# Performance work log

Hardware: AMD Instinct MI355X
Metric: run time of the kernel (lower is better)

The kernel has to match this reference:

```python
import jax, jax.numpy as jnp
import numpy as np
from jax import lax

B, C, T = 16, 1, 2097152
DS = 16  # downsample_factor


def setup_inputs() -> dict:
    key = jax.random.key(0)
    audio = jax.random.normal(key, (B, C, T), dtype=jnp.float32) * 0.5
    sr, attack_ms, release_ms = 44100.0, 10.0, 100.0
    tc = float(np.exp(-np.log10(9.0)))  # exp(-log10(9)) time-constant numerator
    return {
        'audio': audio,
        'threshold': jnp.array([-20.0], jnp.float32),
        'ratio': jnp.array([4.0], jnp.float32),
        'makeup': jnp.array([3.0], jnp.float32),
        'attack_time': jnp.array([tc / (sr * attack_ms * 0.001 * DS)], jnp.float32),
        'release_time': jnp.array([tc / (sr * release_ms * 0.001 * DS)], jnp.float32),
    }


def _linear_downsample(x, factor):
    # F.interpolate(mode='linear', align_corners=False, scale_factor=1/factor)
    Tin = x.shape[-1]
    Tout = Tin // factor
    scale = Tin / Tout
    src = (jnp.arange(Tout, dtype=jnp.float32) + 0.5) * scale - 0.5
    src = jnp.clip(src, 0.0, Tin - 1)
    x0 = jnp.floor(src).astype(jnp.int32)
    x1 = jnp.minimum(x0 + 1, Tin - 1)
    w = src - x0.astype(jnp.float32)
    return x[..., x0] * (1.0 - w) + x[..., x1] * w


def _upsample_with_windows(x, up):
    # x: [B, C, F] framewise envelope; overlap-add with periodic Hann, hop=up
    xb = jnp.concatenate([x, x[..., -1:]], axis=-1)  # add endpoint
    n = jnp.arange(2 * up, dtype=jnp.float32)
    win = 0.5 * (1.0 - jnp.cos(2.0 * jnp.pi * n / (2 * up)))  # torch.hann_window (periodic)
    frames = xb[..., None] * win  # [B, C, F+1, 2*up]
    bsz, ch, nf, fl = frames.shape
    L = (nf - 1) * up + fl
    idx = (jnp.arange(nf)[:, None] * up + jnp.arange(fl)[None, :]).reshape(-1)
    out = jnp.zeros((bsz, ch, L), frames.dtype).at[:, :, idx].add(frames.reshape(bsz, ch, -1))
    return out[:, :, up:-up]


def reference(audio, threshold, ratio, makeup, attack_time, release_time):
    audio_db = 20.0 * jnp.log10(jnp.abs(audio) + 1e-8)
    comp_db = jnp.where(audio_db > threshold,
                        threshold + (audio_db - threshold) / ratio,
                        audio_db)
    gain = comp_db - audio_db  # [B, C, T], static gain reduction in dB (<= 0)
    gd = _linear_downsample(gain, DS)  # [B, C, T//DS]
    # sequential attack/release gain smoothing (one-pole recurrence) over frames
    gd_t = jnp.moveaxis(gd, -1, 0)  # [T//DS, B, C]
    def step(prev, tgt):
        new = jnp.where(tgt >= prev,
                        attack_time * prev + (1.0 - attack_time) * tgt,
                        release_time * prev + (1.0 - release_time) * tgt)
        return new, new
    _, ys = lax.scan(step, gd_t[0], gd_t)
    gs = jnp.moveaxis(ys, 0, -1)  # smoothed gain, [B, C, T//DS]
    gup = _upsample_with_windows(gs, DS)[..., :gain.shape[-1]]
    out_db = audio_db + gup + makeup
    out = 10.0 ** (out_db / 20.0)
    return jnp.where(audio < 0, -out, out)
```

## Files before the change

kernel.cpp:

```cpp
#include <hip/hip_runtime.h>
#include <math.h>

#define B_SZ 16
#define T_LEN 2097152
#define F_LEN (T_LEN / 16)
#define CHUNK 16
#define CPB (F_LEN / CHUNK)
#define NCHUNKS (B_SZ * CPB)
#define NV4 (B_SZ * T_LEN / 4)
#define PRE 16

__device__ __forceinline__ float gain_db(float s, float thr, float slope) {
    float db = 6.0205999132796239f * __log2f(fabsf(s) + 1e-8f);
    float ov = db - thr;
    return ov > 0.0f ? ov * slope : 0.0f;
}

__global__ __launch_bounds__(256) void k_scan(const float* __restrict__ audio,
                                              const float* __restrict__ thr_p,
                                              const float* __restrict__ ratio_p,
                                              const float* __restrict__ at_p,
                                              const float* __restrict__ rt_p,
                                              float2* __restrict__ gsp) {
    int idx = blockIdx.x * 256 + threadIdx.x;
    int b = idx >> 13;
    int c = idx & (CPB - 1);
    int c0 = c << 4;
    const float* Af = audio + (size_t)b * T_LEN;
    const float thr   = thr_p[0];
    const float slope = 1.0f / ratio_p[0] - 1.0f;

    float g[PRE + CHUNK + 1];
#pragma unroll
    for (int i = 0; i < PRE + CHUNK + 1; ++i) {
        int f = c0 - PRE + i;
        f = f < 0 ? 0 : (f > F_LEN - 1 ? F_LEN - 1 : f);
        float t7 = Af[(size_t)f * 16 + 7];
        float t8 = Af[(size_t)f * 16 + 8];
        g[i] = 0.5f * (gain_db(t7, thr, slope) + gain_db(t8, thr, slope));
    }

    const float at = at_p[0], rt = rt_p[0];
    float o[CHUNK + 1];
    float y;
    if (c == 0) {
        y = g[PRE];
        o[0] = y;
#pragma unroll
        for (int i = 1; i < CHUNK + 1; ++i) {
            float t = g[PRE + i];
            y = fmaf((t >= y) ? at : rt, y - t, t);
            o[i] = y;
        }
    } else {
        y = g[0];
#pragma unroll
        for (int i = 1; i < PRE; ++i) {
            float t = g[i];
            y = fmaf((t >= y) ? at : rt, y - t, t);
        }
#pragma unroll
        for (int i = 0; i < CHUNK + 1; ++i) {
            float t = g[PRE + i];
            y = fmaf((t >= y) ? at : rt, y - t, t);
            o[i] = y;
        }
    }
    if (c == CPB - 1) o[CHUNK] = o[CHUNK - 1];

    float2 pr[CHUNK];
#pragma unroll
    for (int i = 0; i < CHUNK; ++i)
        pr[i] = make_float2(o[i], o[i + 1]);
    float4* q4 = reinterpret_cast<float4*>(gsp + (size_t)b * F_LEN + c0);
#pragma unroll
    for (int i = 0; i < CHUNK / 2; ++i)
        q4[i] = reinterpret_cast<float4*>(pr)[i];
}

__global__ __launch_bounds__(256) void k_out(const float4* __restrict__ audio4,
                                             const float2* __restrict__ gsp,
                                             const float* __restrict__ mk_p,
                                             float4* __restrict__ out4) {
    int i = blockIdx.x * 256 + threadIdx.x;
    int t0 = i << 2;
    int b = t0 >> 21;
    int t = t0 & (T_LEN - 1);
    int q = t >> 4;
    int r0 = t & 15;
    float2 gp = gsp[(size_t)b * F_LEN + q];
    float gq = gp.x;
    float d  = gp.y - gp.x;
    const float K   = 0.16609640474436813f;
    const float mkK = mk_p[0] * K;
    float4 x = audio4[i];
    float xs[4] = {x.x, x.y, x.z, x.w};
    float os[4];
#pragma unroll
    for (int j = 0; j < 4; ++j) {
        float cs  = __cosf((float)(r0 + j) * 0.19634954084936207f);
        float wl  = 0.5f - 0.5f * cs;
        float gup = fmaf(d, wl, gq);
        float m   = fabsf(xs[j]) + 1e-8f;
        float v   = m * __builtin_amdgcn_exp2f(fmaf(gup, K, mkK));
        os[j] = (xs[j] < 0.0f) ? -v : v;
    }
    out4[i] = make_float4(os[0], os[1], os[2], os[3]);
}

extern "C" void kernel_launch(void* const* d_in, const int* in_sizes, int n_in,
                              void* d_out, int out_size, void* d_ws, size_t ws_size,
                              hipStream_t stream) {
    const float* audio  = (const float*)d_in[0];
    const float* thr    = (const float*)d_in[1];
    const float* ratio  = (const float*)d_in[2];
    const float* makeup = (const float*)d_in[3];
    const float* at     = (const float*)d_in[4];
    const float* rt     = (const float*)d_in[5];
    float* out = (float*)d_out;

    float2* gsp = (float2*)d_ws;

    k_scan<<<NCHUNKS / 256, 256, 0, stream>>>(audio, thr, ratio, at, rt, gsp);
    k_out<<<NV4 / 256, 256, 0, stream>>>((const float4*)audio, gsp, makeup,
                                         (float4*)out);
}
```

Baseline: 274.9 us.

## Fuse gain scan and output into one kernel with wave-local LDS exchange

Merges the scan and output kernels into one. Each wave loads its 1024 audio samples once, computes frame gains from the held samples using lane shuffles, and runs the chunked recurrence in four lanes with a warm-up prefix through LDS. The output is then applied directly, which removes the global float2 intermediate, a second pass over the audio and one launch. It also replaces the per-sample cosine with precomputed Hann weights. The risks are serialized scan lanes stalling the wave and reliance on wave-level LDS fences instead of __syncthreads.

```diff
diff --git a/kernel.cpp b/kernel.cpp
--- a/kernel.cpp
+++ b/kernel.cpp
@@ -4,108 +4,130 @@
 #define B_SZ 16
 #define T_LEN 2097152
 #define F_LEN (T_LEN / 16)
-#define CHUNK 16
-#define CPB (F_LEN / CHUNK)
-#define NCHUNKS (B_SZ * CPB)
-#define NV4 (B_SZ * T_LEN / 4)
-#define PRE 16
+#define NBLOCKS 8192
+#define K_LOG 0.16609640474436813f
+
+typedef float f32x4 __attribute__((ext_vector_type(4)));
+
+#define KEEP4(v) asm volatile("" :: "v"(v.x), "v"(v.y), "v"(v.z), "v"(v.w))
+#define LGKM_FENCE() asm volatile("s_waitcnt lgkmcnt(0)" ::: "memory")
 
 __device__ __forceinline__ float gain_db(float s, float thr, float slope) {
     float db = 6.0205999132796239f * __log2f(fabsf(s) + 1e-8f);
     float ov = db - thr;
     return ov > 0.0f ? ov * slope : 0.0f;
 }
+__device__ __forceinline__ float step1(float y, float t, float at, float rt) {
+    return fmaf((t >= y) ? at : rt, y - t, t);
+}
+__device__ __forceinline__ float win_sel(int p, float a, float b, float c, float d) {
+    float lo = (p & 1) ? b : a;
+    float hi = (p & 1) ? d : c;
+    return (p & 2) ? hi : lo;
+}
 
-__global__ __launch_bounds__(256) void k_scan(const float* __restrict__ audio,
-                                              const float* __restrict__ thr_p,
-                                              const float* __restrict__ ratio_p,
-                                              const float* __restrict__ at_p,
-                                              const float* __restrict__ rt_p,
-                                              float2* __restrict__ gsp) {
-    int idx = blockIdx.x * 256 + threadIdx.x;
-    int b = idx >> 13;
-    int c = idx & (CPB - 1);
-    int c0 = c << 4;
-    const float* Af = audio + (size_t)b * T_LEN;
+__global__ __launch_bounds__(256) void k_fused(const float4* __restrict__ audio4,
+                                               const float* __restrict__ thr_p,
+                                               const float* __restrict__ ratio_p,
+                                               const float* __restrict__ mk_p,
+                                               const float* __restrict__ at_p,
+                                               const float* __restrict__ rt_p,
+                                               float4* __restrict__ out4) {
+    __shared__ float  gd_s[4][84];
+    __shared__ float2 yp_s[4][64];
+
+    const int tid  = threadIdx.x;
+    const int lane = tid & 63;
+    const int wv   = tid >> 6;
+    const int b    = blockIdx.x >> 9;
+    const int bib  = blockIdx.x & 511;
+    const int W0   = (bib << 8) + (wv << 6);
+
+    const float*  Af = (const float*)audio4 + (size_t)b * T_LEN;
+    const float4* A4 = audio4 + (size_t)b * (T_LEN / 4) + (size_t)W0 * 4;
+    float4*       O4 = out4  + (size_t)b * (T_LEN / 4) + (size_t)W0 * 4;
+
+    float4 xs0 = A4[lane];
+    float4 xs1 = A4[lane + 64];
+    float4 xs2 = A4[lane + 128];
+    float4 xs3 = A4[lane + 192];
+    KEEP4(xs0); KEEP4(xs1); KEEP4(xs2); KEEP4(xs3);
+
+    float t7 = 0.0f, t8 = 0.0f;
+    if (lane < 17) {
+        int fr = (lane < 16) ? (W0 - 16 + lane) : (W0 + 64);
+        fr = fr < 0 ? 0 : (fr > F_LEN - 1 ? F_LEN - 1 : fr);
+        t7 = Af[(size_t)fr * 16 + 7];
+        t8 = Af[(size_t)fr * 16 + 8];
+    }
+
     const float thr   = thr_p[0];
     const float slope = 1.0f / ratio_p[0] - 1.0f;
+    const float at = at_p[0], rt = rt_p[0];
+    const int   p  = lane & 3;
 
-    float g[PRE + CHUNK + 1];
-#pragma unroll
-    for (int i = 0; i < PRE + CHUNK + 1; ++i) {
-        int f = c0 - PRE + i;
-        f = f < 0 ? 0 : (f > F_LEN - 1 ? F_LEN - 1 : f);
-        float t7 = Af[(size_t)f * 16 + 7];
-        float t8 = Af[(size_t)f * 16 + 8];
-        g[i] = 0.5f * (gain_db(t7, thr, slope) + gain_db(t8, thr, slope));
+#define GDJ(J, XV) {                                                   \
+        float v  = (p == 1) ? XV.w : XV.x;                             \
+        float g  = gain_db(v, thr, slope);                             \
+        float gp = __shfl_xor(g, 3);                                   \
+        if (p == 1) gd_s[wv][16 + 16 * J + (lane >> 2)] = 0.5f * (g + gp); }
+    GDJ(0, xs0) GDJ(1, xs1) GDJ(2, xs2) GDJ(3, xs3)
+#undef GDJ
+    if (lane < 17) {
+        float gw = 0.5f * (gain_db(t7, thr, slope) + gain_db(t8, thr, slope));
+        gd_s[wv][(lane < 16) ? lane : 80] = gw;
     }
+    LGKM_FENCE();
 
-    const float at = at_p[0], rt = rt_p[0];
-    float o[CHUNK + 1];
-    float y;
-    if (c == 0) {
-        y = g[PRE];
-        o[0] = y;
-#pragma unroll
-        for (int i = 1; i < CHUNK + 1; ++i) {
-            float t = g[PRE + i];
-            y = fmaf((t >= y) ? at : rt, y - t, t);
-            o[i] = y;
+    if (lane < 4) {
+        const float4* gp4 = reinterpret_cast<const float4*>(&gd_s[wv][16 * lane]);
+        float4 r0 = gp4[0], r1 = gp4[1], r2 = gp4[2], r3 = gp4[3];
+        float4 r4 = gp4[4], r5 = gp4[5], r6 = gp4[6], r7 = gp4[7];
+        float  rE = gd_s[wv][16 * lane + 32];
+        __builtin_amdgcn_sched_barrier(0);
+        bool exact = (bib == 0) && (wv == 0) && (lane == 0);
+        float y;
+        if (exact) {
+            y = r4.x;
+        } else {
+            y = r0.x;
+            y = step1(y, r0.y, at, rt); y = step1(y, r0.z, at, rt); y = step1(y, r0.w, at, rt);
+            y = step1(y, r1.x, at, rt); y = step1(y, r1.y, at, rt); y = step1(y, r1.z, at, rt); y = step1(y, r1.w, at, rt);
+            y = step1(y, r2.x, at, rt); y = step1(y, r2.y, at, rt); y = step1(y, r2.z, at, rt); y = step1(y, r2.w, at, rt);
+            y = step1(y, r3.x, at, rt); y = step1(y, r3.y, at, rt); y = step1(y, r3.z, at, rt); y = step1(y, r3.w, at, rt);
+            y = step1(y, r4.x, at, rt);
         }
-    } else {
-        y = g[0];
-#pragma unroll
-        for (int i = 1; i < PRE; ++i) {
-            float t = g[i];
-            y = fmaf((t >= y) ? at : rt, y - t, t);
-        }
-#pragma unroll
-        for (int i = 0; i < CHUNK + 1; ++i) {
-            float t = g[PRE + i];
-            y = fmaf((t >= y) ? at : rt, y - t, t);
-            o[i] = y;
-        }
+        float2* ypb = &yp_s[wv][16 * lane];
+        float yn;
+#define PAIRSTEP(T, IDX) yn = step1(y, T, at, rt); ypb[IDX] = make_float2(y, yn); y = yn;
+        PAIRSTEP(r4.y, 0)  PAIRSTEP(r4.z, 1)  PAIRSTEP(r4.w, 2)
+        PAIRSTEP(r5.x, 3)  PAIRSTEP(r5.y, 4)  PAIRSTEP(r5.z, 5)  PAIRSTEP(r5.w, 6)
+        PAIRSTEP(r6.x, 7)  PAIRSTEP(r6.y, 8)  PAIRSTEP(r6.z, 9)  PAIRSTEP(r6.w, 10)
+        PAIRSTEP(r7.x, 11) PAIRSTEP(r7.y, 12) PAIRSTEP(r7.z, 13) PAIRSTEP(r7.w, 14)
+        PAIRSTEP(rE, 15)
+#undef PAIRSTEP
     }
-    if (c == CPB - 1) o[CHUNK] = o[CHUNK - 1];
+    LGKM_FENCE();
 
-    float2 pr[CHUNK];
-#pragma unroll
-    for (int i = 0; i < CHUNK; ++i)
-        pr[i] = make_float2(o[i], o[i + 1]);
-    float4* q4 = reinterpret_cast<float4*>(gsp + (size_t)b * F_LEN + c0);
-#pragma unroll
-    for (int i = 0; i < CHUNK / 2; ++i)
-        q4[i] = reinterpret_cast<float4*>(pr)[i];
-}
+    const float mkK = mk_p[0] * K_LOG;
+    const int fsub = lane >> 2;
+    const float wl0 = win_sel(p, 0.0f,                 0.14644660940672624f, 0.5f,                 0.85355339059327376f);
+    const float wl1 = win_sel(p, 0.00960735979838478f, 0.22221488349019889f, 0.59754516100806413f, 0.91573480615127262f);
+    const float wl2 = win_sel(p, 0.03806023374435663f, 0.30865828381745511f, 0.69134171618254489f, 0.96193976625564337f);
+    const float wl3 = win_sel(p, 0.08426519384872738f, 0.40245483899193587f, 0.77778511650980111f, 0.99039264020161522f);
 
-__global__ __launch_bounds__(256) void k_out(const float4* __restrict__ audio4,
-                                             const float2* __restrict__ gsp,
-                                             const float* __restrict__ mk_p,
-                                             float4* __restrict__ out4) {
-    int i = blockIdx.x * 256 + threadIdx.x;
-    int t0 = i << 2;
-    int b = t0 >> 21;
-    int t = t0 & (T_LEN - 1);
-    int q = t >> 4;
-    int r0 = t & 15;
-    float2 gp = gsp[(size_t)b * F_LEN + q];
-    float gq = gp.x;
-    float d  = gp.y - gp.x;
-    const float K   = 0.16609640474436813f;
-    const float mkK = mk_p[0] * K;
-    float4 x = audio4[i];
-    float xs[4] = {x.x, x.y, x.z, x.w};
-    float os[4];
-#pragma unroll
-    for (int j = 0; j < 4; ++j) {
-        float cs  = __cosf((float)(r0 + j) * 0.19634954084936207f);
-        float wl  = 0.5f - 0.5f * cs;
-        float gup = fmaf(d, wl, gq);
-        float m   = fabsf(xs[j]) + 1e-8f;
-        float v   = m * __builtin_amdgcn_exp2f(fmaf(gup, K, mkK));
-        os[j] = (xs[j] < 0.0f) ? -v : v;
-    }
-    out4[i] = make_float4(os[0], os[1], os[2], os[3]);
+#define OUTC(C, WL) { float m = fabsf(C) + 1e-8f;                                   \
+        float vv = m * __builtin_amdgcn_exp2f(fmaf(fmaf(dd, WL, gq), K_LOG, mkK));  \
+        C = (C < 0.0f) ? -vv : vv; }
+#define OUTJ(J, XV) {                                                               \
+        float2 pr = yp_s[wv][16 * J + fsub];                                        \
+        float gq = pr.x;                                                            \
+        float dd = (W0 + 16 * J + fsub == F_LEN - 1) ? 0.0f : (pr.y - pr.x);        \
+        OUTC(XV.x, wl0) OUTC(XV.y, wl1) OUTC(XV.z, wl2) OUTC(XV.w, wl3)             \
+        O4[64 * J + lane] = XV; }
+    OUTJ(0, xs0) OUTJ(1, xs1) OUTJ(2, xs2) OUTJ(3, xs3)
+#undef OUTJ
+#undef OUTC
 }
 
 extern "C" void kernel_launch(void* const* d_in, const int* in_sizes, int n_in,
@@ -117,11 +139,7 @@
     const float* makeup = (const float*)d_in[3];
     const float* at     = (const float*)d_in[4];
     const float* rt     = (const float*)d_in[5];
-    float* out = (float*)d_out;
 
-    float2* gsp = (float2*)d_ws;
-
-    k_scan<<<NCHUNKS / 256, 256, 0, stream>>>(audio, thr, ratio, at, rt, gsp);
-    k_out<<<NV4 / 256, 256, 0, stream>>>((const float4*)audio, gsp, makeup,
-                                         (float4*)out);
+    k_fused<<<NBLOCKS, 256, 0, stream>>>((const float4*)audio, thr, ratio, makeup,
+                                         at, rt, (float4*)d_out);
 }
```

After: 237.9 us. 1.16x faster.
